# Kernel tuning notes

Hardware: AMD Instinct MI355X
Metric: run time of the kernel (lower is better)

The kernel has to match this reference:

```python
import jax, jax.numpy as jnp
import numpy as np
from jax import lax

B_SZ, L, D_MODEL = 2, 2048, 1024
D_INNER, D_STATE, D_CONV, DT_RANK = 2048, 16, 4, 64


def setup_inputs() -> dict:
    key = jax.random.key(0)
    ks = jax.random.split(key, 9)
    s = 0.02
    x = jax.random.normal(ks[0], (B_SZ, L, D_MODEL), dtype=jnp.float32)
    W_in = jax.random.normal(ks[1], (D_MODEL, 2 * D_INNER), dtype=jnp.float32) * s
    conv_w = jax.random.normal(ks[2], (D_INNER, D_CONV), dtype=jnp.float32) * s
    conv_b = jax.random.normal(ks[3], (D_INNER,), dtype=jnp.float32) * s
    W_x = jax.random.normal(ks[4], (D_INNER, DT_RANK + 2 * D_STATE), dtype=jnp.float32) * s
    W_dt = jax.random.normal(ks[5], (DT_RANK, D_INNER), dtype=jnp.float32) * s
    b_dt = jax.random.normal(ks[6], (D_INNER,), dtype=jnp.float32) * s
    A_log = jnp.log(jnp.broadcast_to(jnp.arange(1, D_STATE + 1, dtype=jnp.float32), (D_INNER, D_STATE)))
    D = jnp.ones((D_INNER,), dtype=jnp.float32)
    W_out = jax.random.normal(ks[7], (D_INNER, D_MODEL), dtype=jnp.float32) * s
    return {"x": x, "W_in": W_in, "conv_w": conv_w, "conv_b": conv_b,
            "W_x": W_x, "W_dt": W_dt, "b_dt": b_dt, "A_log": A_log, "D": D, "W_out": W_out}


def _silu(v):
    return v * jax.nn.sigmoid(v)


def _mamba_fwd(x, W_in, conv_w, conv_b, W_x, W_dt, b_dt, A_log, D, W_out):
    b, l, _ = x.shape
    xz = x @ W_in                                  # [b,l,2*d_inner]
    xs, res = jnp.split(xz, 2, axis=-1)
    # causal depthwise conv1d (torch pads d_conv-1 both sides then truncates to l -> left pad only)
    xc = xs.transpose(0, 2, 1)                     # [b,d_inner,l]
    xc = lax.conv_general_dilated(
        xc, conv_w[:, None, :], window_strides=(1,),
        padding=[(D_CONV - 1, 0)], feature_group_count=D_INNER,
        dimension_numbers=("NCH", "OIH", "NCH")) + conv_b[None, :, None]
    u = _silu(xc.transpose(0, 2, 1))               # [b,l,d_inner]
    # projections for delta, B, C
    x_dbl = u @ W_x                                # [b,l,dt_rank+2n]
    dt, Bm, Cm = jnp.split(x_dbl, [DT_RANK, DT_RANK + D_STATE], axis=-1)
    delta = jax.nn.softplus(dt @ W_dt + b_dt)      # [b,l,d_inner]
    A = -jnp.exp(A_log)                            # [d_inner,n]

    def step(h, inp):
        d_t, B_t, C_t, u_t = inp                   # [b,d_in],[b,n],[b,n],[b,d_in]
        dA = jnp.exp(d_t[:, :, None] * A)          # [b,d_in,n]
        h = dA * h + d_t[:, :, None] * B_t[:, None, :] * u_t[:, :, None]
        y = jnp.einsum("bdn,bn->bd", h, C_t)
        return h, y

    h0 = jnp.zeros((b, D_INNER, D_STATE), dtype=u.dtype)
    _, ys = lax.scan(step, h0, (delta.transpose(1, 0, 2), Bm.transpose(1, 0, 2),
                                Cm.transpose(1, 0, 2), u.transpose(1, 0, 2)))
    y = ys.transpose(1, 0, 2) + u * D              # [b,l,d_inner]
    y = y * _silu(res)
    return y @ W_out                               # [b,l,d_model]


def reference(x, W_in, conv_w, conv_b, W_x, W_dt, b_dt, A_log, D, W_out):
    return _mamba_fwd(x, W_in, conv_w, conv_b, W_x, W_dt, b_dt, A_log, D, W_out)
```

## Files before the change

### kernel.cpp

```cpp
#include <hip/hip_runtime.h>
#include <hip/hip_bf16.h>
#include <math.h>

#define B_SZ    2
#define LSEQ    2048
#define DMODEL  1024
#define DINNER  2048
#define DSTATE  16
#define DCONV   4
#define DTRANK  64

#define NCHUNK  64
#define CLEN    (LSEQ / NCHUNK)

#define KSPLIT  8
#define NX      96

typedef unsigned short u16;
typedef __bf16 bf16x8 __attribute__((ext_vector_type(8)));
typedef float  f32x4  __attribute__((ext_vector_type(4)));

static __device__ __forceinline__ float sigmoidf_(float x) {
    return 1.0f / (1.0f + __expf(-x));
}
static __device__ __forceinline__ u16 f2b(float f) {
    unsigned int u = __float_as_uint(f);
    u = (u + 0x7fffu + ((u >> 16) & 1u)) >> 16;
    return (u16)u;
}
static __device__ __forceinline__ float b2f(u16 v) {
    return __uint_as_float(((unsigned int)v) << 16);
}

static __device__ __forceinline__ void xcd_swizzle(int& bx, int& by) {
    const int gx  = gridDim.x;
    const int lin = by * gx + bx;
    const int cpx = (gx * gridDim.y) >> 3;
    const int wg  = (lin & 7) * cpx + (lin >> 3);
    bx = wg % gx;  by = wg / gx;
}

__global__ __launch_bounds__(256) void cast_bf16(
    const float* __restrict__ in, u16* __restrict__ out, int n8)
{
    const int i = blockIdx.x * 256 + threadIdx.x;
    if (i >= n8) return;
    const float4* p = reinterpret_cast<const float4*>(in + (size_t)i * 8);
    float4 v0 = p[0], v1 = p[1];
    union { u16 u[8]; uint4 q; } r;
    r.u[0] = f2b(v0.x); r.u[1] = f2b(v0.y); r.u[2] = f2b(v0.z); r.u[3] = f2b(v0.w);
    r.u[4] = f2b(v1.x); r.u[5] = f2b(v1.y); r.u[6] = f2b(v1.z); r.u[7] = f2b(v1.w);
    reinterpret_cast<uint4*>(out)[i] = r.q;
}

__global__ __launch_bounds__(256) void castT_bf16(
    const float* __restrict__ in, u16* __restrict__ out, int R, int C)
{
    __shared__ float t[32][33];
    const int r0 = blockIdx.y * 32, c0 = blockIdx.x * 32;
    const int tr = threadIdx.x >> 3;
    const int tc4 = (threadIdx.x & 7) * 4;
    const float4 v = *reinterpret_cast<const float4*>(in + (size_t)(r0 + tr) * C + c0 + tc4);
    t[tr][tc4 + 0] = v.x; t[tr][tc4 + 1] = v.y; t[tr][tc4 + 2] = v.z; t[tr][tc4 + 3] = v.w;
    __syncthreads();
    union { u16 u[4]; uint2 q; } r;
    #pragma unroll
    for (int j = 0; j < 4; j++) r.u[j] = f2b(t[tc4 + j][tr]);
    *reinterpret_cast<uint2*>(out + (size_t)(c0 + tr) * R + r0 + tc4) = r.q;
}

__global__ __launch_bounds__(512, 1) void gemm1_8ph(
    const u16* __restrict__ A, const u16* __restrict__ Bt,
    u16* __restrict__ xs_bf, u16* __restrict__ zs_bf)
{
    extern __shared__ u16 smem[];
    const int tid  = threadIdx.x;
    const int lane = tid & 63;
    const int wave = tid >> 6;
    const int wr = wave >> 2, wc = wave & 3;
    int bxs = blockIdx.x, bys = blockIdx.y;
    xcd_swizzle(bxs, bys);
    const int bm = bys * 256, bn = bxs * 256;
    const int lhi = lane >> 4, llo = lane & 15;
    constexpr int K  = DMODEL;
    constexpr int NT = K / 64;

    const int lrow8 = lane >> 3;
    const int gsrc  = ((lane & 7) ^ lrow8) * 8;

    f32x4 acc[8][4] = {};

    auto stage = [&](int kt, int buf) {
        #pragma unroll
        for (int h = 0; h < 2; ++h)
            #pragma unroll
            for (int i = 0; i < 2; ++i) {
                const int rowb = h * 128 + i * 64 + wave * 8;
                const int o16  = buf * 16384 + h * 8192 + i * 4096 + wave * 512;
                const u16* ga = A + (size_t)(bm + rowb + lrow8) * K + kt * 64 + gsrc;
                __builtin_amdgcn_global_load_lds(
                    (const __attribute__((address_space(1))) void*)ga,
                    (__attribute__((address_space(3))) void*)(smem + o16), 16, 0, 0);
                const u16* gb = Bt + (size_t)(bn + rowb + lrow8) * K + kt * 64 + gsrc;
                __builtin_amdgcn_global_load_lds(
                    (const __attribute__((address_space(1))) void*)gb,
                    (__attribute__((address_space(3))) void*)(smem + 32768 + o16), 16, 0, 0);
            }
    };
    auto lda = [&](int m, int ks, int buf) -> bf16x8 {
        const int row = wr * 128 + m * 16 + llo;
        const int g   = (ks * 4 + lhi) ^ (llo & 7);
        return *reinterpret_cast<const bf16x8*>(smem + buf * 16384 + row * 64 + g * 8);
    };
    auto ldb = [&](int n, int ks, int buf) -> bf16x8 {
        const int row = wc * 64 + n * 16 + llo;
        const int g   = (ks * 4 + lhi) ^ (llo & 7);
        return *reinterpret_cast<const bf16x8*>(smem + 32768 + buf * 16384 + row * 64 + g * 8);
    };

    stage(0, 0);
    stage(1, 1);
    asm volatile("s_waitcnt vmcnt(8)" ::: "memory");
    __builtin_amdgcn_s_barrier();

    #pragma unroll 2
    for (int t = 0; t < NT; ++t) {
        const int cur = t & 1;
        bf16x8 afr[4][2], bf0[2][2], bf1[2][2];

        #pragma unroll
        for (int m = 0; m < 4; ++m) { afr[m][0] = lda(m, 0, cur); afr[m][1] = lda(m, 1, cur); }
        #pragma unroll
        for (int n = 0; n < 2; ++n) { bf0[n][0] = ldb(n, 0, cur); bf0[n][1] = ldb(n, 1, cur); }
        __builtin_amdgcn_s_setprio(1);
        #pragma unroll
        for (int m = 0; m < 4; ++m)
            #pragma unroll
            for (int n = 0; n < 2; ++n) {
                acc[m][n] = __builtin_amdgcn_mfma_f32_16x16x32_bf16(afr[m][0], bf0[n][0], acc[m][n], 0, 0, 0);
                acc[m][n] = __builtin_amdgcn_mfma_f32_16x16x32_bf16(afr[m][1], bf0[n][1], acc[m][n], 0, 0, 0);
            }
        __builtin_amdgcn_s_setprio(0);

        #pragma unroll
        for (int n = 0; n < 2; ++n) { bf1[n][0] = ldb(2 + n, 0, cur); bf1[n][1] = ldb(2 + n, 1, cur); }
        __builtin_amdgcn_s_setprio(1);
        #pragma unroll
        for (int m = 0; m < 4; ++m)
            #pragma unroll
            for (int n = 0; n < 2; ++n) {
                acc[m][2 + n] = __builtin_amdgcn_mfma_f32_16x16x32_bf16(afr[m][0], bf1[n][0], acc[m][2 + n], 0, 0, 0);
                acc[m][2 + n] = __builtin_amdgcn_mfma_f32_16x16x32_bf16(afr[m][1], bf1[n][1], acc[m][2 + n], 0, 0, 0);
            }
        __builtin_amdgcn_s_setprio(0);

        #pragma unroll
        for (int m = 0; m < 4; ++m) { afr[m][0] = lda(4 + m, 0, cur); afr[m][1] = lda(4 + m, 1, cur); }
        __builtin_amdgcn_s_setprio(1);
        #pragma unroll
        for (int m = 0; m < 4; ++m)
            #pragma unroll
            for (int n = 0; n < 2; ++n) {
                acc[4 + m][2 + n] = __builtin_amdgcn_mfma_f32_16x16x32_bf16(afr[m][0], bf1[n][0], acc[4 + m][2 + n], 0, 0, 0);
                acc[4 + m][2 + n] = __builtin_amdgcn_mfma_f32_16x16x32_bf16(afr[m][1], bf1[n][1], acc[4 + m][2 + n], 0, 0, 0);
            }
        __builtin_amdgcn_s_setprio(0);

        __builtin_amdgcn_sched_barrier(0);
        __builtin_amdgcn_s_barrier();
        __builtin_amdgcn_sched_barrier(0);

        if (t + 2 < NT) stage(t + 2, cur);
        __builtin_amdgcn_s_setprio(1);
        #pragma unroll
        for (int m = 0; m < 4; ++m)
            #pragma unroll
            for (int n = 0; n < 2; ++n) {
                acc[4 + m][n] = __builtin_amdgcn_mfma_f32_16x16x32_bf16(afr[m][0], bf0[n][0], acc[4 + m][n], 0, 0, 0);
                acc[4 + m][n] = __builtin_amdgcn_mfma_f32_16x16x32_bf16(afr[m][1], bf0[n][1], acc[4 + m][n], 0, 0, 0);
            }
        __builtin_amdgcn_s_setprio(0);

        __builtin_amdgcn_sched_barrier(0);
        if (t + 2 < NT) { asm volatile("s_waitcnt vmcnt(8)" ::: "memory"); }
        else            { asm volatile("s_waitcnt vmcnt(0)" ::: "memory"); }
        __builtin_amdgcn_s_barrier();
        __builtin_amdgcn_sched_barrier(0);
    }

    const bool is_xs = (bn < DINNER);
    #pragma unroll
    for (int m = 0; m < 8; ++m) {
        const int row0 = bm + wr * 128 + m * 16 + lhi * 4;
        #pragma unroll
        for (int n = 0; n < 4; ++n) {
            const int col = bn + wc * 64 + n * 16 + llo;
            #pragma unroll
            for (int j = 0; j < 4; ++j) {
                float v = acc[m][n][j];
                if (is_xs) {
                    xs_bf[(size_t)(row0 + j) * DINNER + col] = f2b(v);
                } else {
                    v = v * sigmoidf_(v);
                    zs_bf[(size_t)(row0 + j) * DINNER + (col - DINNER)] = f2b(v);
                }
            }
        }
    }
}

template<int EPI>
__global__ __launch_bounds__(256) void gemm_mfma(
    const u16* __restrict__ A, const u16* __restrict__ Bt,
    float* __restrict__ Cf, u16* __restrict__ o0, u16* __restrict__ o1,
    const float* __restrict__ bias, int M, int N, int K, int ldc)
{
    __shared__ u16 As[128 * 32];
    __shared__ u16 Bs[128 * 32];
    const int tid  = threadIdx.x;
    const int lane = tid & 63;
    const int wave = tid >> 6;
    const int wr = wave >> 1, wc = wave & 1;
    int bxs = blockIdx.x, bys = blockIdx.y;
    xcd_swizzle(bxs, bys);
    const int bm = bys * 128, bn = bxs * 128;
    const int lhi = lane >> 4;
    const int llo = lane & 15;

    f32x4 acc[4][4] = {};

    const int rs = (lhi ^ ((llo >> 1) & 3)) * 8;

    for (int k0 = 0; k0 < K; k0 += 32) {
        #pragma unroll
        for (int c = 0; c < 2; ++c) {
            const int s   = c * 256 + wave * 64 + lane;
            const int row = s >> 2, seg = s & 3;
            const int sseg = seg ^ ((row >> 1) & 3);
            const u16* ga = A  + (size_t)(bm + row) * K + k0 + sseg * 8;
            const u16* gb = Bt + (size_t)(bn + row) * K + k0 + sseg * 8;
            __builtin_amdgcn_global_load_lds(
                (const __attribute__((address_space(1))) void*)ga,
                (__attribute__((address_space(3))) void*)(As + (size_t)(c * 256 + wave * 64) * 8),
                16, 0, 0);
            __builtin_amdgcn_global_load_lds(
                (const __attribute__((address_space(1))) void*)gb,
                (__attribute__((address_space(3))) void*)(Bs + (size_t)(c * 256 + wave * 64) * 8),
                16, 0, 0);
        }
        __syncthreads();

        bf16x8 af[4], bfr[4];
        #pragma unroll
        for (int m = 0; m < 4; ++m)
            af[m] = *reinterpret_cast<const bf16x8*>(&As[(wr * 64 + m * 16 + llo) * 32 + rs]);
        #pragma unroll
        for (int n = 0; n < 4; ++n)
            bfr[n] = *reinterpret_cast<const bf16x8*>(&Bs[(wc * 64 + n * 16 + llo) * 32 + rs]);
        #pragma unroll
        for (int m = 0; m < 4; ++m)
            #pragma unroll
            for (int n = 0; n < 4; ++n)
                acc[m][n] = __builtin_amdgcn_mfma_f32_16x16x32_bf16(af[m], bfr[n], acc[m][n], 0, 0, 0);
        __syncthreads();
    }

    #pragma unroll
    for (int m = 0; m < 4; ++m) {
        const int row0 = bm + wr * 64 + m * 16 + lhi * 4;
        #pragma unroll
        for (int n = 0; n < 4; ++n) {
            const int col = bn + wc * 64 + n * 16 + llo;
            #pragma unroll
            for (int j = 0; j < 4; ++j) {
                float v = acc[m][n][j];
                if (EPI == 0) {
                    Cf[(size_t)(row0 + j) * ldc + col] = v;
                } else {
                    v += bias[col];
                    v = (v > 20.f) ? v : log1pf(__expf(v));
                    o0[(size_t)(row0 + j) * ldc + col] = f2b(v);
                }
            }
        }
    }
}

__global__ __launch_bounds__(256) void conv_silu_bf(
    const u16* __restrict__ xs, const float* __restrict__ conv_w,
    const float* __restrict__ conv_b, u16* __restrict__ u)
{
    const int g  = blockIdx.x * 256 + threadIdx.x;
    const int d8 = (g & 255) * 8;
    const int bl = g >> 8;
    const int l  = bl & (LSEQ - 1);

    float4 wv[8];
    #pragma unroll
    for (int j = 0; j < 8; j++)
        wv[j] = *reinterpret_cast<const float4*>(conv_w + (size_t)(d8 + j) * DCONV);

    float acc[8];
    #pragma unroll
    for (int j = 0; j < 8; j++) acc[j] = conv_b[d8 + j];

    #pragma unroll
    for (int k = 0; k < DCONV; k++) {
        const int l2 = l - (DCONV - 1) + k;
        if (l2 < 0) continue;
        const uint4 q = *reinterpret_cast<const uint4*>(
            xs + (size_t)(bl - (DCONV - 1) + k) * DINNER + d8);
        const u16* e = reinterpret_cast<const u16*>(&q);
        #pragma unroll
        for (int j = 0; j < 8; j++) {
            const float w = (k == 0) ? wv[j].x : (k == 1) ? wv[j].y : (k == 2) ? wv[j].z : wv[j].w;
            acc[j] = fmaf(b2f(e[j]), w, acc[j]);
        }
    }
    union { u16 u[8]; uint4 q; } r;
    #pragma unroll
    for (int j = 0; j < 8; j++) {
        const float v = acc[j];
        r.u[j] = f2b(v * sigmoidf_(v));
    }
    *reinterpret_cast<uint4*>(u + (size_t)bl * DINNER + d8) = r.q;
}

__global__ __launch_bounds__(256) void gemm3_splitk(
    const u16* __restrict__ ubf, const float* __restrict__ Wx,
    float* __restrict__ partial)
{
    __shared__ float us[64][65];
    __shared__ float wsm[64][96];

    const int tid = threadIdx.x;
    const int r0 = blockIdx.x * 64;
    const int k0 = blockIdx.y * (DINNER / KSPLIT);

    const int orow = tid >> 2;
    const int oc0  = (tid & 3) * 24;

    float acc[24];
    #pragma unroll
    for (int j = 0; j < 24; j++) acc[j] = 0.f;

    for (int ks = 0; ks < DINNER / KSPLIT; ks += 64) {
        {
            const int row = tid >> 2;
            const int c16 = (tid & 3) << 4;
            const uint4* src = reinterpret_cast<const uint4*>(
                ubf + (size_t)(r0 + row) * DINNER + k0 + ks + c16);
            const uint4 q0 = src[0], q1 = src[1];
            const u16* e0 = reinterpret_cast<const u16*>(&q0);
            const u16* e1 = reinterpret_cast<const u16*>(&q1);
            #pragma unroll
            for (int j = 0; j < 8; j++) us[row][c16 + j]     = b2f(e0[j]);
            #pragma unroll
            for (int j = 0; j < 8; j++) us[row][c16 + 8 + j] = b2f(e1[j]);
        }
        #pragma unroll
        for (int j = 0; j < 6; j++) {
            const int fid = tid + j * 256;
            const int kr  = fid / 24;
            const int c4  = (fid % 24) * 4;
            *reinterpret_cast<float4*>(&wsm[kr][c4]) =
                *reinterpret_cast<const float4*>(Wx + (size_t)(k0 + ks + kr) * NX + c4);
        }
        __syncthreads();

        for (int kk = 0; kk < 64; ++kk) {
            const float uv = us[orow][kk];
            #pragma unroll
            for (int j = 0; j < 24; j++)
                acc[j] = fmaf(uv, wsm[kk][oc0 + j], acc[j]);
        }
        __syncthreads();
    }

    float* pp = partial + ((size_t)blockIdx.y * (B_SZ * LSEQ) + r0 + orow) * NX + oc0;
    #pragma unroll
    for (int j = 0; j < 24; j += 4)
        *reinterpret_cast<float4*>(pp + j) = make_float4(acc[j], acc[j+1], acc[j+2], acc[j+3]);
}

__global__ __launch_bounds__(256) void gemm3_reduce(
    const float* __restrict__ partial, float* __restrict__ xdbl,
    u16* __restrict__ x64bf)
{
    const int i = blockIdx.x * 256 + threadIdx.x;
    if (i >= B_SZ * LSEQ * NX / 4) return;
    float4 s = make_float4(0.f, 0.f, 0.f, 0.f);
    #pragma unroll
    for (int p = 0; p < KSPLIT; p++) {
        const float4 v = reinterpret_cast<const float4*>(
            partial + (size_t)p * (B_SZ * LSEQ) * NX)[i];
        s.x += v.x; s.y += v.y; s.z += v.z; s.w += v.w;
    }
    reinterpret_cast<float4*>(xdbl)[i] = s;

    const int col4 = (i % 24) * 4;
    if (col4 < DTRANK) {
        const int row = i / 24;
        union { u16 u[4]; uint2 q; } r;
        r.u[0] = f2b(s.x); r.u[1] = f2b(s.y); r.u[2] = f2b(s.z); r.u[3] = f2b(s.w);
        *reinterpret_cast<uint2*>(x64bf + (size_t)row * DTRANK + col4) = r.q;
    }
}

__global__ __launch_bounds__(256) void scan_phase1(
    const u16* __restrict__ dl_bf, const u16* __restrict__ ubf,
    const float* __restrict__ xdbl, const float* __restrict__ A_log,
    float* __restrict__ hend, float* __restrict__ Sd)
{
    const int idx = blockIdx.x * 256 + threadIdx.x;
    const int d = idx & (DINNER - 1);
    const int c = (idx >> 11) & (NCHUNK - 1);
    const int b = idx >> 17;

    float a[DSTATE];
    #pragma unroll
    for (int n = 0; n < DSTATE; n++) a[n] = -__expf(A_log[d * DSTATE + n]);

    float h[DSTATE];
    #pragma unroll
    for (int n = 0; n < DSTATE; n++) h[n] = 0.f;
    float sd = 0.f;

    const int l0 = b * LSEQ + c * CLEN;
    for (int i = 0; i < CLEN; ++i) {
        const size_t r = (size_t)(l0 + i);
        const float dv = b2f(dl_bf[r * DINNER + d]);
        const float uv = b2f(ubf[r * DINNER + d]);
        sd += dv;
        float Bv[DSTATE];
        {
            const float4* bp = reinterpret_cast<const float4*>(xdbl + r * NX + DTRANK);
            float4 q;
            q = bp[0]; Bv[0]=q.x;  Bv[1]=q.y;  Bv[2]=q.z;  Bv[3]=q.w;
            q = bp[1]; Bv[4]=q.x;  Bv[5]=q.y;  Bv[6]=q.z;  Bv[7]=q.w;
            q = bp[2]; Bv[8]=q.x;  Bv[9]=q.y;  Bv[10]=q.z; Bv[11]=q.w;
            q = bp[3]; Bv[12]=q.x; Bv[13]=q.y; Bv[14]=q.z; Bv[15]=q.w;
        }
        const float du = dv * uv;
        #pragma unroll
        for (int n = 0; n < DSTATE; n++)
            h[n] = fmaf(__expf(dv * a[n]), h[n], du * Bv[n]);
    }

    float* hp = hend + ((size_t)(b * DINNER + d) * NCHUNK + c) * DSTATE;
    #pragma unroll
    for (int n = 0; n < DSTATE; n += 4)
        *reinterpret_cast<float4*>(hp + n) = make_float4(h[n], h[n+1], h[n+2], h[n+3]);
    Sd[(size_t)(b * DINNER + d) * NCHUNK + c] = sd;
}

__global__ __launch_bounds__(256) void scan_phase2(
    float* __restrict__ hend, const float* __restrict__ Sd,
    const float* __restrict__ A_log)
{
    const int idx = blockIdx.x * 256 + threadIdx.x;
    if (idx >= B_SZ * DINNER * DSTATE) return;
    const int n = idx & (DSTATE - 1);
    const int d = (idx >> 4) & (DINNER - 1);
    const int b = idx >> 15;

    const float an = -__expf(A_log[d * DSTATE + n]);
    const size_t base = (size_t)(b * DINNER + d) * NCHUNK;
    float carry = 0.f;
    for (int c = 0; c < NCHUNK; ++c) {
        const float P = __expf(an * Sd[base + c]);
        const size_t off = (base + c) * DSTATE + n;
        const float tmp = hend[off];
        hend[off] = carry;
        carry = fmaf(P, carry, tmp);
    }
}

__global__ __launch_bounds__(256) void scan_phase3(
    const u16* __restrict__ dl_bf, const u16* __restrict__ ubf,
    const u16* __restrict__ zs_bf, const float* __restrict__ xdbl,
    const float* __restrict__ A_log, const float* __restrict__ Dp,
    const float* __restrict__ hin, u16* __restrict__ ybf)
{
    const int idx = blockIdx.x * 256 + threadIdx.x;
    const int d = idx & (DINNER - 1);
    const int c = (idx >> 11) & (NCHUNK - 1);
    const int b = idx >> 17;

    float a[DSTATE];
    #pragma unroll
    for (int n = 0; n < DSTATE; n++) a[n] = -__expf(A_log[d * DSTATE + n]);
    const float Dd = Dp[d];

    float h[DSTATE];
    {
        const float* hp = hin + ((size_t)(b * DINNER + d) * NCHUNK + c) * DSTATE;
        #pragma unroll
        for (int n = 0; n < DSTATE; n += 4) {
            const float4 t = *reinterpret_cast<const float4*>(hp + n);
            h[n] = t.x; h[n+1] = t.y; h[n+2] = t.z; h[n+3] = t.w;
        }
    }

    const int l0 = b * LSEQ + c * CLEN;
    for (int i = 0; i < CLEN; ++i) {
        const size_t r = (size_t)(l0 + i);
        const float dv = b2f(dl_bf[r * DINNER + d]);
        const float uv = b2f(ubf[r * DINNER + d]);

        const float4* bp = reinterpret_cast<const float4*>(xdbl + r * NX + DTRANK);
        float Bv[DSTATE], Cv[DSTATE];
        {
            float4 t;
            t = bp[0]; Bv[0]=t.x;  Bv[1]=t.y;  Bv[2]=t.z;  Bv[3]=t.w;
            t = bp[1]; Bv[4]=t.x;  Bv[5]=t.y;  Bv[6]=t.z;  Bv[7]=t.w;
            t = bp[2]; Bv[8]=t.x;  Bv[9]=t.y;  Bv[10]=t.z; Bv[11]=t.w;
            t = bp[3]; Bv[12]=t.x; Bv[13]=t.y; Bv[14]=t.z; Bv[15]=t.w;
            t = bp[4]; Cv[0]=t.x;  Cv[1]=t.y;  Cv[2]=t.z;  Cv[3]=t.w;
            t = bp[5]; Cv[4]=t.x;  Cv[5]=t.y;  Cv[6]=t.z;  Cv[7]=t.w;
            t = bp[6]; Cv[8]=t.x;  Cv[9]=t.y;  Cv[10]=t.z; Cv[11]=t.w;
            t = bp[7]; Cv[12]=t.x; Cv[13]=t.y; Cv[14]=t.z; Cv[15]=t.w;
        }

        const float du = dv * uv;
        float yv = 0.f;
        #pragma unroll
        for (int n = 0; n < DSTATE; n++) {
            h[n] = fmaf(__expf(dv * a[n]), h[n], du * Bv[n]);
            yv = fmaf(h[n], Cv[n], yv);
        }
        yv = fmaf(uv, Dd, yv);

        const float g = b2f(zs_bf[r * DINNER + d]);
        ybf[r * DINNER + d] = f2b(yv * g);
    }
}

extern "C" void kernel_launch(void* const* d_in, const int* in_sizes, int n_in,
                              void* d_out, int out_size, void* d_ws, size_t ws_size,
                              hipStream_t stream) {
    const float* x      = (const float*)d_in[0];
    const float* W_in   = (const float*)d_in[1];
    const float* conv_w = (const float*)d_in[2];
    const float* conv_b = (const float*)d_in[3];
    const float* W_x    = (const float*)d_in[4];
    const float* W_dt   = (const float*)d_in[5];
    const float* b_dt   = (const float*)d_in[6];
    const float* A_log  = (const float*)d_in[7];
    const float* Dp     = (const float*)d_in[8];
    const float* W_out  = (const float*)d_in[9];
    float* out = (float*)d_out;

    const int M = B_SZ * LSEQ;

    float* ws     = (float*)d_ws;
    float* xdbl   = ws;
    float* hend   = xdbl + (size_t)M * NX;
    float* Sd     = hend + (size_t)B_SZ * DINNER * NCHUNK * DSTATE;
    float* part   = Sd   + (size_t)B_SZ * DINNER * NCHUNK;
    u16*   xs_bf  = (u16*)(part + (size_t)KSPLIT * M * NX);
    u16*   zs_bf  = xs_bf + (size_t)M * DINNER;
    u16*   u_bf   = zs_bf + (size_t)M * DINNER;
    u16*   dl_bf  = u_bf  + (size_t)M * DINNER;
    u16*   xbf    = dl_bf + (size_t)M * DINNER;
    u16*   WinT   = xbf   + (size_t)M * DMODEL;
    u16*   WoutT  = WinT  + (size_t)M * DMODEL;
    u16*   x64bf  = WoutT + (size_t)DMODEL * DINNER;
    u16*   WdtT   = x64bf + (size_t)M * DTRANK;
    u16*   ybf    = xbf;

    dim3 blk(256);

    cast_bf16<<<dim3((M * DMODEL / 8) / 256), blk, 0, stream>>>(x, xbf, M * DMODEL / 8);
    castT_bf16<<<dim3((2 * DINNER) / 32, DMODEL / 32), blk, 0, stream>>>(
        W_in, WinT, DMODEL, 2 * DINNER);

    gemm1_8ph<<<dim3((2 * DINNER) / 256, M / 256), dim3(512), 131072, stream>>>(
        xbf, WinT, xs_bf, zs_bf);

    conv_silu_bf<<<dim3((M * DINNER / 8) / 256), blk, 0, stream>>>(
        xs_bf, conv_w, conv_b, u_bf);

    gemm3_splitk<<<dim3(M / 64, KSPLIT), blk, 0, stream>>>(u_bf, W_x, part);
    gemm3_reduce<<<dim3((M * NX / 4 + 255) / 256), blk, 0, stream>>>(part, xdbl, x64bf);

    castT_bf16<<<dim3(DINNER / 32, DTRANK / 32), blk, 0, stream>>>(
        W_dt, WdtT, DTRANK, DINNER);
    gemm_mfma<2><<<dim3(DINNER / 128, M / 128), blk, 0, stream>>>(
        x64bf, WdtT, nullptr, dl_bf, nullptr, b_dt, M, DINNER, DTRANK, DINNER);

    scan_phase1<<<dim3((B_SZ * DINNER * NCHUNK) / 256), blk, 0, stream>>>(
        dl_bf, u_bf, xdbl, A_log, hend, Sd);
    scan_phase2<<<dim3((B_SZ * DINNER * DSTATE) / 256), blk, 0, stream>>>(
        hend, Sd, A_log);
    scan_phase3<<<dim3((B_SZ * DINNER * NCHUNK) / 256), blk, 0, stream>>>(
        dl_bf, u_bf, zs_bf, xdbl, A_log, Dp, hend, ybf);

    castT_bf16<<<dim3(DMODEL / 32, DINNER / 32), blk, 0, stream>>>(
        W_out, WoutT, DINNER, DMODEL);

    gemm_mfma<0><<<dim3(DMODEL / 128, M / 128), blk, 0, stream>>>(
        ybf, WoutT, out, nullptr, nullptr, nullptr, M, DMODEL, DINNER, DMODEL);
}
```

Measured before the change: 387.3 us.

## Merge cast kernels, split-K output GEMM with atomics, separate scan carry buffer

Folds the four fp32-to-bf16 cast/transpose launches into one prep kernel. The final output GEMM is split along K into two slices that accumulate into a zeroed output with atomic adds, which doubles the block count on a grid that only had 256 blocks. Scan phase 2 now writes carries to a separate buffer instead of updating in place, and its loop is unrolled. The changes add a memset and atomic traffic, and the output summation order is no longer deterministic.

```diff
diff --git a/kernel.cpp b/kernel.cpp
--- a/kernel.cpp
+++ b/kernel.cpp
@@ -40,26 +40,13 @@
     bx = wg % gx;  by = wg / gx;
 }
 
-__global__ __launch_bounds__(256) void cast_bf16(
-    const float* __restrict__ in, u16* __restrict__ out, int n8)
-{
-    const int i = blockIdx.x * 256 + threadIdx.x;
-    if (i >= n8) return;
-    const float4* p = reinterpret_cast<const float4*>(in + (size_t)i * 8);
-    float4 v0 = p[0], v1 = p[1];
-    union { u16 u[8]; uint4 q; } r;
-    r.u[0] = f2b(v0.x); r.u[1] = f2b(v0.y); r.u[2] = f2b(v0.z); r.u[3] = f2b(v0.w);
-    r.u[4] = f2b(v1.x); r.u[5] = f2b(v1.y); r.u[6] = f2b(v1.z); r.u[7] = f2b(v1.w);
-    reinterpret_cast<uint4*>(out)[i] = r.q;
-}
-
-__global__ __launch_bounds__(256) void castT_bf16(
-    const float* __restrict__ in, u16* __restrict__ out, int R, int C)
-{
-    __shared__ float t[32][33];
-    const int r0 = blockIdx.y * 32, c0 = blockIdx.x * 32;
-    const int tr = threadIdx.x >> 3;
-    const int tc4 = (threadIdx.x & 7) * 4;
+static __device__ __forceinline__ void castT_body(
+    const float* __restrict__ in, u16* __restrict__ out, int R, int C,
+    int bx, int by, float t[32][33], int tid)
+{
+    const int r0 = by * 32, c0 = bx * 32;
+    const int tr = tid >> 3;
+    const int tc4 = (tid & 7) * 4;
     const float4 v = *reinterpret_cast<const float4*>(in + (size_t)(r0 + tr) * C + c0 + tc4);
     t[tr][tc4 + 0] = v.x; t[tr][tc4 + 1] = v.y; t[tr][tc4 + 2] = v.z; t[tr][tc4 + 3] = v.w;
     __syncthreads();
@@ -67,6 +54,35 @@
     #pragma unroll
     for (int j = 0; j < 4; j++) r.u[j] = f2b(t[tc4 + j][tr]);
     *reinterpret_cast<uint2*>(out + (size_t)(c0 + tr) * R + r0 + tc4) = r.q;
+}
+
+__global__ __launch_bounds__(256) void prep_casts(
+    const float* __restrict__ x,     u16* __restrict__ xbf,
+    const float* __restrict__ W_in,  u16* __restrict__ WinT,
+    const float* __restrict__ W_dt,  u16* __restrict__ WdtT,
+    const float* __restrict__ W_out, u16* __restrict__ WoutT)
+{
+    __shared__ float t[32][33];
+    const int b = blockIdx.x;
+    const int tid = threadIdx.x;
+    if (b < 2048) {
+        const int i = b * 256 + tid;
+        const float4* p = reinterpret_cast<const float4*>(x + (size_t)i * 8);
+        float4 v0 = p[0], v1 = p[1];
+        union { u16 u[8]; uint4 q; } r;
+        r.u[0] = f2b(v0.x); r.u[1] = f2b(v0.y); r.u[2] = f2b(v0.z); r.u[3] = f2b(v0.w);
+        r.u[4] = f2b(v1.x); r.u[5] = f2b(v1.y); r.u[6] = f2b(v1.z); r.u[7] = f2b(v1.w);
+        reinterpret_cast<uint4*>(xbf)[i] = r.q;
+    } else if (b < 6144) {
+        const int lb = b - 2048;
+        castT_body(W_in, WinT, DMODEL, 2 * DINNER, lb % 128, lb / 128, t, tid);
+    } else if (b < 6272) {
+        const int lb = b - 6144;
+        castT_body(W_dt, WdtT, DTRANK, DINNER, lb % 64, lb / 64, t, tid);
+    } else {
+        const int lb = b - 6272;
+        castT_body(W_out, WoutT, DINNER, DMODEL, lb % 32, lb / 32, t, tid);
+    }
 }
 
 __global__ __launch_bounds__(512, 1) void gemm1_8ph(
@@ -212,8 +228,8 @@
 template<int EPI>
 __global__ __launch_bounds__(256) void gemm_mfma(
     const u16* __restrict__ A, const u16* __restrict__ Bt,
-    float* __restrict__ Cf, u16* __restrict__ o0, u16* __restrict__ o1,
-    const float* __restrict__ bias, int M, int N, int K, int ldc)
+    float* __restrict__ Cf, u16* __restrict__ o0,
+    const float* __restrict__ bias, int M, int N, int Klen, int Kstride, int ldc)
 {
     __shared__ u16 As[128 * 32];
     __shared__ u16 Bs[128 * 32];
@@ -224,6 +240,7 @@
     int bxs = blockIdx.x, bys = blockIdx.y;
     xcd_swizzle(bxs, bys);
     const int bm = bys * 128, bn = bxs * 128;
+    const int koff = blockIdx.z * Klen;
     const int lhi = lane >> 4;
     const int llo = lane & 15;
 
@@ -231,14 +248,14 @@
 
     const int rs = (lhi ^ ((llo >> 1) & 3)) * 8;
 
-    for (int k0 = 0; k0 < K; k0 += 32) {
+    for (int k0 = 0; k0 < Klen; k0 += 32) {
         #pragma unroll
         for (int c = 0; c < 2; ++c) {
             const int s   = c * 256 + wave * 64 + lane;
             const int row = s >> 2, seg = s & 3;
             const int sseg = seg ^ ((row >> 1) & 3);
-            const u16* ga = A  + (size_t)(bm + row) * K + k0 + sseg * 8;
-            const u16* gb = Bt + (size_t)(bn + row) * K + k0 + sseg * 8;
+            const u16* ga = A  + (size_t)(bm + row) * Kstride + koff + k0 + sseg * 8;
+            const u16* gb = Bt + (size_t)(bn + row) * Kstride + koff + k0 + sseg * 8;
             __builtin_amdgcn_global_load_lds(
                 (const __attribute__((address_space(1))) void*)ga,
                 (__attribute__((address_space(3))) void*)(As + (size_t)(c * 256 + wave * 64) * 8),
@@ -274,8 +291,8 @@
             #pragma unroll
             for (int j = 0; j < 4; ++j) {
                 float v = acc[m][n][j];
-                if (EPI == 0) {
-                    Cf[(size_t)(row0 + j) * ldc + col] = v;
+                if (EPI == 3) {
+                    unsafeAtomicAdd(&Cf[(size_t)(row0 + j) * ldc + col], v);
                 } else {
                     v += bias[col];
                     v = (v > 20.f) ? v : log1pf(__expf(v));
@@ -455,8 +472,8 @@
 }
 
 __global__ __launch_bounds__(256) void scan_phase2(
-    float* __restrict__ hend, const float* __restrict__ Sd,
-    const float* __restrict__ A_log)
+    const float* __restrict__ hend, float* __restrict__ hin,
+    const float* __restrict__ Sd, const float* __restrict__ A_log)
 {
     const int idx = blockIdx.x * 256 + threadIdx.x;
     if (idx >= B_SZ * DINNER * DSTATE) return;
@@ -467,12 +484,12 @@
     const float an = -__expf(A_log[d * DSTATE + n]);
     const size_t base = (size_t)(b * DINNER + d) * NCHUNK;
     float carry = 0.f;
+    #pragma unroll 4
     for (int c = 0; c < NCHUNK; ++c) {
         const float P = __expf(an * Sd[base + c]);
         const size_t off = (base + c) * DSTATE + n;
-        const float tmp = hend[off];
-        hend[off] = carry;
-        carry = fmaf(P, carry, tmp);
+        hin[off] = carry;
+        carry = fmaf(P, carry, hend[off]);
     }
 }
 
@@ -556,7 +573,8 @@
     float* ws     = (float*)d_ws;
     float* xdbl   = ws;
     float* hend   = xdbl + (size_t)M * NX;
-    float* Sd     = hend + (size_t)B_SZ * DINNER * NCHUNK * DSTATE;
+    float* hin    = hend + (size_t)B_SZ * DINNER * NCHUNK * DSTATE;
+    float* Sd     = hin  + (size_t)B_SZ * DINNER * NCHUNK * DSTATE;
     float* part   = Sd   + (size_t)B_SZ * DINNER * NCHUNK;
     u16*   xs_bf  = (u16*)(part + (size_t)KSPLIT * M * NX);
     u16*   zs_bf  = xs_bf + (size_t)M * DINNER;
@@ -571,9 +589,10 @@
 
     dim3 blk(256);
 
-    cast_bf16<<<dim3((M * DMODEL / 8) / 256), blk, 0, stream>>>(x, xbf, M * DMODEL / 8);
-    castT_bf16<<<dim3((2 * DINNER) / 32, DMODEL / 32), blk, 0, stream>>>(
-        W_in, WinT, DMODEL, 2 * DINNER);
+    prep_casts<<<dim3(8320), blk, 0, stream>>>(
+        x, xbf, W_in, WinT, W_dt, WdtT, W_out, WoutT);
+
+    hipMemsetAsync(out, 0, (size_t)M * DMODEL * sizeof(float), stream);
 
     gemm1_8ph<<<dim3((2 * DINNER) / 256, M / 256), dim3(512), 131072, stream>>>(
         xbf, WinT, xs_bf, zs_bf);
@@ -584,21 +603,16 @@
     gemm3_splitk<<<dim3(M / 64, KSPLIT), blk, 0, stream>>>(u_bf, W_x, part);
     gemm3_reduce<<<dim3((M * NX / 4 + 255) / 256), blk, 0, stream>>>(part, xdbl, x64bf);
 
-    castT_bf16<<<dim3(DINNER / 32, DTRANK / 32), blk, 0, stream>>>(
-        W_dt, WdtT, DTRANK, DINNER);
-    gemm_mfma<2><<<dim3(DINNER / 128, M / 128), blk, 0, stream>>>(
-        x64bf, WdtT, nullptr, dl_bf, nullptr, b_dt, M, DINNER, DTRANK, DINNER);
+    gemm_mfma<2><<<dim3(DINNER / 128, M / 128, 1), blk, 0, stream>>>(
+        x64bf, WdtT, nullptr, dl_bf, b_dt, M, DINNER, DTRANK, DTRANK, DINNER);
 
     scan_phase1<<<dim3((B_SZ * DINNER * NCHUNK) / 256), blk, 0, stream>>>(
         dl_bf, u_bf, xdbl, A_log, hend, Sd);
-    scan_phase2<<<dim3((B_SZ * DINNER * DSTATE) / 256), blk, 0, stream>>>(
-        hend, Sd, A_log);
+    scan_phase2<<<dim3((B_SZ * DINNER * DSTATE + 255) / 256), blk, 0, stream>>>(
+        hend, hin, Sd, A_log);
     scan_phase3<<<dim3((B_SZ * DINNER * NCHUNK) / 256), blk, 0, stream>>>(
-        dl_bf, u_bf, zs_bf, xdbl, A_log, Dp, hend, ybf);
-
-    castT_bf16<<<dim3(DMODEL / 32, DINNER / 32), blk, 0, stream>>>(
-        W_out, WoutT, DINNER, DMODEL);
-
-    gemm_mfma<0><<<dim3(DMODEL / 128, M / 128), blk, 0, stream>>>(
-        ybf, WoutT, out, nullptr, nullptr, nullptr, M, DMODEL, DINNER, DMODEL);
-}
+        dl_bf, u_bf, zs_bf, xdbl, A_log, Dp, hin, ybf);
+
+    gemm_mfma<3><<<dim3(DMODEL / 128, M / 128, 2), blk, 0, stream>>>(
+        ybf, WoutT, out, nullptr, nullptr, M, DMODEL, DINNER / 2, DINNER, DMODEL);
+}
```

New measurement: 391.4 us. No clear change (+1.1%).
